# Performance work log

Measured on AMD Instinct MI355X. Metric: run time of the kernel, lower is better.

Reference implementation:

```python
import jax, jax.numpy as jnp
import numpy as np

B, N, M = 2, 2048, 1024
C, CTX, H = 1024, 1024, 16
D = C // H
HID = int(C * 4.0)
EPS = 1e-6


def _ln(h):
    # LayerNorm32: fp32 layernorm, eps=1e-6, no affine params
    h32 = h.astype(jnp.float32)
    mu = jnp.mean(h32, axis=-1, keepdims=True)
    var = jnp.var(h32, axis=-1, keepdims=True)
    return ((h32 - mu) * jax.lax.rsqrt(var + EPS)).astype(h.dtype)


def _sdpa(q, k, v):
    # q: [B,Q,H,D], k/v: [B,K,H,D]
    scale = 1.0 / np.sqrt(D)
    s = jnp.einsum('bqhd,bkhd->bhqk', q, k) * scale
    p = jax.nn.softmax(s, axis=-1)
    return jnp.einsum('bhqk,bkhd->bqhd', p, v)


def _forward(x, context, Wqkv, bqkv, Wos, bos, Wq, bq, Wkv, bkv, Woc, boc, W1, b1, W2, b2):
    Bx, Nx, _ = x.shape
    Mx = context.shape[1]
    # --- self-attention (attn_mode='full') ---
    h = _ln(x)
    qkv = (h @ Wqkv + bqkv).reshape(Bx, Nx, 3, H, D)
    q, k, v = qkv[:, :, 0], qkv[:, :, 1], qkv[:, :, 2]
    a = _sdpa(q, k, v).reshape(Bx, Nx, C)
    x = x + (a @ Wos + bos)
    # --- cross-attention (always 'full') ---
    h = _ln(x)
    q = (h @ Wq + bq).reshape(Bx, Nx, H, D)
    kv = (context @ Wkv + bkv).reshape(Bx, Mx, 2, H, D)
    k, v = kv[:, :, 0], kv[:, :, 1]
    a = _sdpa(q, k, v).reshape(Bx, Nx, C)
    x = x + (a @ Woc + boc)
    # --- FFN with tanh-approx GELU ---
    h = _ln(x)
    x = x + (jax.nn.gelu(h @ W1 + b1, approximate=True) @ W2 + b2)
    return x


def setup_inputs() -> dict:
    key = jax.random.key(0)
    ks = jax.random.split(key, 12)
    rn = lambda k, shape: (jax.random.normal(k, shape, jnp.float32) * 0.02)
    return {
        'x': jax.random.normal(ks[0], (B, N, C), jnp.float32),
        'context': jax.random.normal(ks[1], (B, M, CTX), jnp.float32),
        'Wqkv': rn(ks[2], (C, 3 * C)), 'bqkv': jnp.zeros((3 * C,), jnp.float32),
        'Wos': rn(ks[3], (C, C)), 'bos': jnp.zeros((C,), jnp.float32),
        'Wq': rn(ks[4], (C, C)), 'bq': jnp.zeros((C,), jnp.float32),
        'Wkv': rn(ks[5], (CTX, 2 * C)), 'bkv': jnp.zeros((2 * C,), jnp.float32),
        'Woc': rn(ks[6], (C, C)), 'boc': jnp.zeros((C,), jnp.float32),
        'W1': rn(ks[7], (C, HID)), 'b1': jnp.zeros((HID,), jnp.float32),
        'W2': rn(ks[8], (HID, C)), 'b2': jnp.zeros((C,), jnp.float32),
    }


def reference(x, context, Wqkv, bqkv, Wos, bos, Wq, bq, Wkv, bkv, Woc, boc, W1, b1, W2, b2):
    return _forward(x, context, Wqkv, bqkv, Wos, bos, Wq, bq, Wkv, bkv, Woc, boc, W1, b1, W2, b2)
```

## Files before the change

kernel.cpp:

```cpp
#include <hip/hip_runtime.h>
#include <cstdint>

typedef unsigned short u16;
typedef short bf16x8 __attribute__((ext_vector_type(8)));
typedef unsigned short u16x8 __attribute__((ext_vector_type(8)));
typedef float f32x4 __attribute__((ext_vector_type(4)));

__device__ __forceinline__ u16 f2bf(float f) {
  union { float f; uint32_t u; } v; v.f = f;
  uint32_t r = (v.u + 0x7fffu + ((v.u >> 16) & 1u)) >> 16;
  return (u16)r;
}

__device__ __forceinline__ void gload_lds16(const u16* g, u16* l) {
  __builtin_amdgcn_global_load_lds(
      (const __attribute__((address_space(1))) void*)g,
      (__attribute__((address_space(3))) void*)l, 16, 0, 0);
}

__global__ __launch_bounds__(256) void ln_kernel(const float* __restrict__ x,
                                                 u16* __restrict__ h) {
  const int row = blockIdx.x;
  const int tid = threadIdx.x;
  const float4 v = *reinterpret_cast<const float4*>(x + (long)row * 1024 + tid * 4);
  float s  = v.x + v.y + v.z + v.w;
  float ss = v.x * v.x + v.y * v.y + v.z * v.z + v.w * v.w;
#pragma unroll
  for (int off = 32; off >= 1; off >>= 1) {
    s  += __shfl_xor(s, off, 64);
    ss += __shfl_xor(ss, off, 64);
  }
  __shared__ float red[8];
  const int wave = tid >> 6, lane = tid & 63;
  if (lane == 0) { red[wave] = s; red[4 + wave] = ss; }
  __syncthreads();
  s  = red[0] + red[1] + red[2] + red[3];
  ss = red[4] + red[5] + red[6] + red[7];
  const float mu   = s * (1.0f / 1024.0f);
  const float var  = ss * (1.0f / 1024.0f) - mu * mu;
  const float rstd = rsqrtf(var + 1e-6f);
  ushort4 o;
  o.x = f2bf((v.x - mu) * rstd);
  o.y = f2bf((v.y - mu) * rstd);
  o.z = f2bf((v.z - mu) * rstd);
  o.w = f2bf((v.w - mu) * rstd);
  *reinterpret_cast<ushort4*>(h + (long)row * 1024 + tid * 4) = o;
}

struct WEnt { const float* W; u16* Wt; int K, N, tEnd; };
struct WEnts { WEnt e[7]; int n; };

__global__ __launch_bounds__(256) void wconvert_all(WEnts args) {
  __shared__ u16 tile[64][72];
  int t = blockIdx.x;
  int i = 0, tStart = 0;
  while (i < args.n - 1 && t >= args.e[i].tEnd) { tStart = args.e[i].tEnd; i++; }
  const float* W = args.e[i].W;
  u16* Wt = args.e[i].Wt;
  const int K = args.e[i].K, N = args.e[i].N;
  const int rel = t - tStart;
  const int ntn = N >> 6;
  const int tn = rel % ntn, tk = rel / ntn;
  const int n0 = tn * 64, k0 = tk * 64;

  const int th = threadIdx.x;
  const int c4 = (th & 15) * 4;
  const int r  = th >> 4;
#pragma unroll
  for (int ii = 0; ii < 4; ii++) {
    const int row = ii * 16 + r;
    const float4 v = *reinterpret_cast<const float4*>(W + (long)(k0 + row) * N + n0 + c4);
    tile[c4 + 0][row] = f2bf(v.x);
    tile[c4 + 1][row] = f2bf(v.y);
    tile[c4 + 2][row] = f2bf(v.z);
    tile[c4 + 3][row] = f2bf(v.w);
  }
  __syncthreads();
  const int c8 = (th & 7) * 8;
  const int rn = th >> 3;
#pragma unroll
  for (int ii = 0; ii < 2; ii++) {
    const int row = ii * 32 + rn;
    *reinterpret_cast<u16x8*>(Wt + (long)(n0 + row) * K + k0 + c8) =
        *reinterpret_cast<const u16x8*>(&tile[row][c8]);
  }
}

__global__ __launch_bounds__(256) void f2bf_kernel(const float* __restrict__ in,
                                                   u16* __restrict__ out) {
  const long i = ((long)blockIdx.x * 256 + threadIdx.x) * 4;
  const float4 v = *reinterpret_cast<const float4*>(in + i);
  ushort4 o;
  o.x = f2bf(v.x); o.y = f2bf(v.y); o.z = f2bf(v.z); o.w = f2bf(v.w);
  *reinterpret_cast<ushort4*>(out + i) = o;
}

__global__ __launch_bounds__(256) void vtrans(const u16* __restrict__ V,
                                              u16* __restrict__ Vt,
                                              int vStride, long vBatch, int nk) {
  __shared__ u16 tile[64][72];
  const int t = threadIdx.x;
  const int b = blockIdx.z, h = blockIdx.y, n0 = blockIdx.x * 64;
  const u16* vp = V + (long)b * vBatch + h * 64;
  u16* op = Vt + (long)(b * 16 + h) * 64 * (long)nk + n0;
  const int ch = t & 7;
#pragma unroll
  for (int i = 0; i < 2; i++) {
    const int n = (t >> 3) + i * 32;
    const u16x8 v = *reinterpret_cast<const u16x8*>(vp + (long)(n0 + n) * vStride + ch * 8);
#pragma unroll
    for (int j = 0; j < 8; j++) tile[ch * 8 + j][n] = v[j];
  }
  __syncthreads();
#pragma unroll
  for (int i = 0; i < 2; i++) {
    const int d = (t >> 3) + i * 32;
    *reinterpret_cast<u16x8*>(op + (long)d * nk + ch * 8) =
        *reinterpret_cast<const u16x8*>(&tile[d][ch * 8]);
  }
}

template <int TN, bool OUT_BF16, bool GELU_ACT, bool RES, int KSPLIT>
__device__ __forceinline__ void gemm_core(
    const u16* __restrict__ A, const u16* __restrict__ Bt,
    const float* __restrict__ bias, const float* __restrict__ res,
    void* __restrict__ Cout, int Ndim, int Kdim, int m0, int n0,
    u16* Al, u16* Bl) {
  constexpr int NFRAG = TN / 32;
  const int tid  = threadIdx.x;
  const int lane = tid & 63, wave = tid >> 6;
  const int quad = lane >> 4, l15 = lane & 15;
  const int wr = wave >> 1, wc = wave & 1;

  f32x4 acc[4][NFRAG];
  const f32x4 vzero = {0.f, 0.f, 0.f, 0.f};
#pragma unroll
  for (int i = 0; i < 4; i++)
#pragma unroll
    for (int jj = 0; jj < NFRAG; jj++) acc[i][jj] = vzero;

  const int Keff = Kdim / KSPLIT;
  const long kOff = (KSPLIT > 1) ? (long)blockIdx.y * Keff : 0;

  const long rowOff = (long)(lane >> 2) * Kdim + (((lane & 3) ^ ((lane >> 3) & 3)) * 8);
  const u16* gA = A  + (long)m0 * Kdim + rowOff + kOff;
  const u16* gB = Bt + (long)n0 * Kdim + rowOff + kOff;

  auto stage = [&](int k0, int p) {
    gload_lds16(gA + (long)(wave * 16) * Kdim + k0,       Al + p * 4096 + wave * 512);
    gload_lds16(gA + (long)((wave + 4) * 16) * Kdim + k0, Al + p * 4096 + (wave + 4) * 512);
    gload_lds16(gB + (long)(wave * 16) * Kdim + k0,       Bl + p * (TN * 32) + wave * 512);
    if constexpr (TN == 128)
      gload_lds16(gB + (long)((wave + 4) * 16) * Kdim + k0, Bl + p * (TN * 32) + (wave + 4) * 512);
  };

  const int swz = (quad ^ ((l15 >> 1) & 3)) * 8;

  stage(0, 0);
  int p = 0;
  for (int k0 = 0; k0 < Keff; k0 += 32, p ^= 1) {
    __syncthreads();
    bf16x8 af[4], bfr[NFRAG];
#pragma unroll
    for (int mt = 0; mt < 4; mt++)
      af[mt] = *reinterpret_cast<const bf16x8*>(Al + p * 4096 + (wr * 64 + mt * 16 + l15) * 32 + swz);
#pragma unroll
    for (int nt = 0; nt < NFRAG; nt++)
      bfr[nt] = *reinterpret_cast<const bf16x8*>(Bl + p * (TN * 32) + (wc * NFRAG * 16 + nt * 16 + l15) * 32 + swz);
    if (k0 + 32 < Keff) stage(k0 + 32, p ^ 1);
#pragma unroll
    for (int mt = 0; mt < 4; mt++)
#pragma unroll
      for (int nt = 0; nt < NFRAG; nt++)
        acc[mt][nt] = __builtin_amdgcn_mfma_f32_16x16x32_bf16(af[mt], bfr[nt], acc[mt][nt], 0, 0, 0);
  }

#pragma unroll
  for (int nt = 0; nt < NFRAG; nt++) {
    const int col = n0 + wc * NFRAG * 16 + nt * 16 + l15;
    const float bv = bias[col];
#pragma unroll
    for (int mt = 0; mt < 4; mt++) {
#pragma unroll
      for (int r = 0; r < 4; r++) {
        const int row = m0 + wr * 64 + mt * 16 + quad * 4 + r;
        if constexpr (KSPLIT > 1) {
          float y = acc[mt][nt][r];
          if (blockIdx.y == 0) y += bv;
          unsafeAtomicAdd(&((float*)Cout)[(long)row * Ndim + col], y);
        } else {
          float y = acc[mt][nt][r] + bv;
          if (GELU_ACT) {
            const float t = 0.7978845608028654f * (y + 0.044715f * y * y * y);
            y = 0.5f * y * (1.0f + tanhf(t));
          }
          if (RES) y += res[(long)row * Ndim + col];
          if (OUT_BF16)
            ((u16*)Cout)[(long)row * Ndim + col] = f2bf(y);
          else
            ((float*)Cout)[(long)row * Ndim + col] = y;
        }
      }
    }
  }
}

template <int TN, int SX, bool OUT_BF16, bool GELU_ACT, bool RES, int KSPLIT = 1>
__global__ __launch_bounds__(256, 2) void gemm_bt(
    const u16* __restrict__ A, const u16* __restrict__ Bt,
    const float* __restrict__ bias, const float* __restrict__ res,
    void* __restrict__ Cout, int Ndim, int Kdim, int lx, int ly) {
  __shared__ u16 Al[2 * 128 * 32];
  __shared__ u16 Bl[2 * TN * 32];
  const int j = blockIdx.x;
  const int c = j & 7, kk = j >> 3;
  const int cx = c % SX, cy = c / SX;
  const int bx = cx * lx + (kk % lx);
  const int by = cy * ly + (kk / lx);
  gemm_core<TN, OUT_BF16, GELU_ACT, RES, KSPLIT>(
      A, Bt, bias, res, Cout, Ndim, Kdim, by * 128, bx * TN, Al, Bl);
}

struct GemmSeg {
  const u16* A; const u16* Bt; const float* bias; u16* C;
  int Ndim, Kdim, SX, lx, ly;
};
struct GemmDualP { GemmSeg s0, s1; int nBlk0; };

template <int TN>
__global__ __launch_bounds__(256, 2) void gemm_dual(GemmDualP pp) {
  __shared__ u16 Al[2 * 128 * 32];
  __shared__ u16 Bl[2 * TN * 32];
  int j = blockIdx.x;
  GemmSeg s;
  if (j < pp.nBlk0) { s = pp.s0; } else { s = pp.s1; j -= pp.nBlk0; }
  const int c = j & 7, kk = j >> 3;
  const int cx = c % s.SX, cy = c / s.SX;
  const int bx = cx * s.lx + (kk % s.lx);
  const int by = cy * s.ly + (kk / s.lx);
  gemm_core<TN, true, false, false, 1>(
      s.A, s.Bt, s.bias, nullptr, s.C, s.Ndim, s.Kdim, by * 128, bx * TN, Al, Bl);
}

__global__ __launch_bounds__(256, 2) void attn_kernel(
    const u16* __restrict__ Q, const u16* __restrict__ K, const u16* __restrict__ Vt,
    u16* __restrict__ O, int nk, int qStride, int kStride, int oStride,
    long qBatch, long kBatch, long oBatch) {
  __shared__ u16 Kt[2][64 * 64];
  __shared__ u16 Vl[2][64 * 64];
  __shared__ u16 Pl[4][32 * 64];

  const int tid = threadIdx.x;
  const int lane = tid & 63, wave = tid >> 6;
  const int quad = lane >> 4, l15 = lane & 15;
  const int b = blockIdx.z, hh = blockIdx.y, qt = blockIdx.x;

  const u16* qp = Q + (long)b * qBatch + hh * 64;
  const u16* kp = K + (long)b * kBatch + hh * 64;
  const u16* vp = Vt + (long)(b * 16 + hh) * 64 * (long)nk;

  bf16x8 qf[2][2];
  const int qrow = qt * 128 + wave * 32 + l15;
#pragma unroll
  for (int qg = 0; qg < 2; qg++) {
    qf[qg][0] = *reinterpret_cast<const bf16x8*>(qp + (long)(qrow + qg * 16) * qStride + quad * 8);
    qf[qg][1] = *reinterpret_cast<const bf16x8*>(qp + (long)(qrow + qg * 16) * qStride + 32 + quad * 8);
  }

  const int r8 = lane >> 3;
  const int gcol = ((lane & 7) ^ r8) * 8;
  const u16* kgA = kp + (long)(wave * 8 + r8) * kStride + gcol;
  const u16* kgB = kp + (long)((wave + 4) * 8 + r8) * kStride + gcol;
  const u16* vgA = vp + (long)(wave * 8 + r8) * nk + gcol;
  const u16* vgB = vp + (long)((wave + 4) * 8 + r8) * nk + gcol;

  const int cF = (quad ^ (l15 & 7)) * 8;

  const f32x4 vzero = {0.f, 0.f, 0.f, 0.f};
  f32x4 oAcc[2][4];
  float lSt[2] = {0.f, 0.f};
#pragma unroll
  for (int qg = 0; qg < 2; qg++)
#pragma unroll
    for (int i = 0; i < 4; i++) oAcc[qg][i] = vzero;

  const float SCL = 0.18033688f;
  const int nTiles = nk >> 6;
  const long kAdv = (long)64 * kStride;

  auto stage = [&](int kt, int p) {
    gload_lds16(kgA + kt * kAdv, &Kt[p][wave * 512]);
    gload_lds16(kgB + kt * kAdv, &Kt[p][(wave + 4) * 512]);
    gload_lds16(vgA + kt * 64,   &Vl[p][wave * 512]);
    gload_lds16(vgB + kt * 64,   &Vl[p][(wave + 4) * 512]);
  };

  stage(0, 0);
  int p = 0;
  for (int kt = 0; kt < nTiles; kt++, p ^= 1) {
    __syncthreads();
    if (kt + 1 < nTiles) stage(kt + 1, p ^ 1);

    f32x4 st[2][4];
#pragma unroll
    for (int mt = 0; mt < 4; mt++) {
      const bf16x8 kf0 = *reinterpret_cast<const bf16x8*>(&Kt[p][(mt * 16 + l15) * 64 + cF]);
      const bf16x8 kf1 = *reinterpret_cast<const bf16x8*>(&Kt[p][(mt * 16 + l15) * 64 + (cF ^ 32)]);
#pragma unroll
      for (int qg = 0; qg < 2; qg++) {
        f32x4 z = vzero;
        z = __builtin_amdgcn_mfma_f32_16x16x32_bf16(kf0, qf[qg][0], z, 0, 0, 0);
        z = __builtin_amdgcn_mfma_f32_16x16x32_bf16(kf1, qf[qg][1], z, 0, 0, 0);
        st[qg][mt] = z;
      }
    }

#pragma unroll
    for (int qg = 0; qg < 2; qg++) {
      float ps = 0.f;
#pragma unroll
      for (int mt = 0; mt < 4; mt++)
#pragma unroll
        for (int r = 0; r < 4; r++) {
          const float pw = __builtin_amdgcn_exp2f(st[qg][mt][r] * SCL);
          st[qg][mt][r] = pw;
          ps += pw;
        }
      lSt[qg] += ps;
      u16* plw = &Pl[wave][(qg * 16 + l15) * 64];
#pragma unroll
      for (int mt = 0; mt < 4; mt++) {
        union { float f; uint32_t u; } a0, a1, a2, a3;
        a0.f = st[qg][mt][0]; a1.f = st[qg][mt][1];
        a2.f = st[qg][mt][2]; a3.f = st[qg][mt][3];
        a0.u += 0x8000u; a1.u += 0x8000u; a2.u += 0x8000u; a3.u += 0x8000u;
        uint2 w;
        w.x = __builtin_amdgcn_perm(a1.u, a0.u, 0x07060302u);
        w.y = __builtin_amdgcn_perm(a3.u, a2.u, 0x07060302u);
        const int pcol = (((mt * 2 + (quad >> 1)) ^ (l15 & 7)) * 8) + (quad & 1) * 4;
        *reinterpret_cast<uint2*>(&plw[pcol]) = w;
      }
    }

    bf16x8 pf[2][2];
#pragma unroll
    for (int qg = 0; qg < 2; qg++) {
      const u16* plw = &Pl[wave][(qg * 16 + l15) * 64];
      pf[qg][0] = *reinterpret_cast<const bf16x8*>(&plw[cF]);
      pf[qg][1] = *reinterpret_cast<const bf16x8*>(&plw[cF ^ 32]);
    }
#pragma unroll
    for (int dt = 0; dt < 4; dt++) {
      const bf16x8 vf0 = *reinterpret_cast<const bf16x8*>(&Vl[p][(dt * 16 + l15) * 64 + cF]);
      const bf16x8 vf1 = *reinterpret_cast<const bf16x8*>(&Vl[p][(dt * 16 + l15) * 64 + (cF ^ 32)]);
#pragma unroll
      for (int qg = 0; qg < 2; qg++) {
        oAcc[qg][dt] = __builtin_amdgcn_mfma_f32_16x16x32_bf16(pf[qg][0], vf0, oAcc[qg][dt], 0, 0, 0);
        oAcc[qg][dt] = __builtin_amdgcn_mfma_f32_16x16x32_bf16(pf[qg][1], vf1, oAcc[qg][dt], 0, 0, 0);
      }
    }
  }

  u16* op = O + (long)b * oBatch + hh * 64;
#pragma unroll
  for (int qg = 0; qg < 2; qg++) {
    float l = lSt[qg];
    l += __shfl_xor(l, 16, 64);
    l += __shfl_xor(l, 32, 64);
    float lR[4];
#pragma unroll
    for (int r = 0; r < 4; r++) lR[r] = 1.0f / __shfl(l, quad * 4 + r, 64);
#pragma unroll
    for (int dt = 0; dt < 4; dt++)
#pragma unroll
      for (int r = 0; r < 4; r++) {
        const int row = qt * 128 + wave * 32 + qg * 16 + quad * 4 + r;
        op[(long)row * oStride + dt * 16 + l15] = f2bf(oAcc[qg][dt][r] * lR[r]);
      }
  }
}

extern "C" void kernel_launch(void* const* d_in, const int* in_sizes, int n_in,
                              void* d_out, int out_size, void* d_ws, size_t ws_size,
                              hipStream_t stream) {
  const float* x    = (const float*)d_in[0];
  const float* ctx  = (const float*)d_in[1];
  const float* Wqkv = (const float*)d_in[2];
  const float* bqkv = (const float*)d_in[3];
  const float* Wos  = (const float*)d_in[4];
  const float* bos  = (const float*)d_in[5];
  const float* Wq   = (const float*)d_in[6];
  const float* bq   = (const float*)d_in[7];
  const float* Wkv  = (const float*)d_in[8];
  const float* bkv  = (const float*)d_in[9];
  const float* Woc  = (const float*)d_in[10];
  const float* boc  = (const float*)d_in[11];
  const float* W1   = (const float*)d_in[12];
  const float* b1   = (const float*)d_in[13];
  const float* W2   = (const float*)d_in[14];
  const float* b2   = (const float*)d_in[15];
  float* out = (float*)d_out;
  char* ws = (char*)d_ws;
  const size_t MB = 1024 * 1024;

  u16* h      = (u16*)ws;
  u16* abuf   = (u16*)(ws + 8 * MB);
  u16* wbuf   = (u16*)(ws + 8 * MB);
  u16* qkv    = (u16*)(ws + 16 * MB);
  u16* Wqkvt  = (u16*)(ws + 40 * MB);
  u16* Wost   = (u16*)(ws + 16 * MB);
  u16* Wqt    = (u16*)(ws + 18 * MB);
  u16* Wkvt   = (u16*)(ws + 20 * MB);
  u16* Woct   = (u16*)(ws + 24 * MB);
  u16* q2     = (u16*)(ws + 26 * MB);
  u16* kv2    = (u16*)(ws + 34 * MB);
  u16* ctxbf  = (u16*)(ws + 42 * MB);
  u16* VtCr   = (u16*)(ws + 16 * MB);
  u16* hid    = (u16*)(ws + 16 * MB);
  u16* VtSelf = h;
  u16* W1t    = wbuf;
  u16* W2t    = wbuf;

  WEnts w1; w1.n = 1;

  ln_kernel<<<dim3(4096), dim3(256), 0, stream>>>(x, h);
  w1.e[0] = {Wqkv, Wqkvt, 1024, 3072, 768};
  wconvert_all<<<dim3(768), dim3(256), 0, stream>>>(w1);
  gemm_bt<128, 2, true, false, false><<<dim3(768), dim3(256), 0, stream>>>(
      h, Wqkvt, bqkv, nullptr, qkv, 3072, 1024, 12, 8);
  vtrans<<<dim3(32, 16, 2), dim3(256), 0, stream>>>(
      qkv + 2048, VtSelf, 3072, (long)2048 * 3072, 2048);
  attn_kernel<<<dim3(16, 16, 2), dim3(256), 0, stream>>>(
      qkv, qkv + 1024, VtSelf, abuf, 2048, 3072, 3072, 1024,
      (long)2048 * 3072, (long)2048 * 3072, (long)2048 * 1024);

  WEnts w4; w4.n = 4;
  w4.e[0] = {Wos, Wost, 1024, 1024, 256};
  w4.e[1] = {Wq,  Wqt,  1024, 1024, 512};
  w4.e[2] = {Wkv, Wkvt, 1024, 2048, 1024};
  w4.e[3] = {Woc, Woct, 1024, 1024, 1280};
  wconvert_all<<<dim3(1280), dim3(256), 0, stream>>>(w4);
  f2bf_kernel<<<dim3(2048), dim3(256), 0, stream>>>(ctx, ctxbf);

  gemm_bt<64, 1, false, false, true><<<dim3(512), dim3(256), 0, stream>>>(
      abuf, Wost, bos, x, out, 1024, 1024, 16, 4);
  ln_kernel<<<dim3(4096), dim3(256), 0, stream>>>(out, h);

  GemmDualP dp;
  dp.s0 = {h,     Wqt,  bq,  q2,  1024, 1024, 1, 16, 4};
  dp.s1 = {ctxbf, Wkvt, bkv, kv2, 2048, 1024, 2, 16, 4};
  dp.nBlk0 = 512;
  gemm_dual<64><<<dim3(1024), dim3(256), 0, stream>>>(dp);
  vtrans<<<dim3(16, 16, 2), dim3(256), 0, stream>>>(
      kv2 + 1024, VtCr, 2048, (long)1024 * 2048, 1024);
  attn_kernel<<<dim3(16, 16, 2), dim3(256), 0, stream>>>(
      q2, kv2, VtCr, abuf, 1024, 1024, 2048, 1024,
      (long)2048 * 1024, (long)1024 * 2048, (long)2048 * 1024);
  gemm_bt<64, 1, false, false, false, 2><<<dim3(512, 2), dim3(256), 0, stream>>>(
      abuf, Woct, boc, nullptr, out, 1024, 1024, 16, 4);

  ln_kernel<<<dim3(4096), dim3(256), 0, stream>>>(out, h);
  w1.e[0] = {W1, W1t, 1024, 4096, 1024};
  wconvert_all<<<dim3(1024), dim3(256), 0, stream>>>(w1);
  gemm_bt<128, 2, true, true, false><<<dim3(1024), dim3(256), 0, stream>>>(
      h, W1t, b1, nullptr, hid, 4096, 1024, 16, 8);
  w1.e[0] = {W2, W2t, 4096, 1024, 1024};
  wconvert_all<<<dim3(1024), dim3(256), 0, stream>>>(w1);
  gemm_bt<128, 2, false, false, false, 4><<<dim3(256, 4), dim3(256), 0, stream>>>(
      hid, W2t, b2, nullptr, out, 1024, 4096, 4, 8);
}
```

Before: 520.9 us.

## Fuse layernorm with weight conversion, drop split-K atomics, use exp2 GELU

Merges the layernorm and weight-conversion launches into combined grids, and merges the context bf16 conversion with the weight-conversion launch, to cut launch count and let independent work overlap. Removes split-K with atomic adds for the cross-attention output projection and the FFN down projection. Those now use a single-pass 64-wide tile GEMM that adds the residual in place, which avoids atomic traffic but gives fewer blocks on the K=4096 GEMM. Replaces tanhf in GELU with an exp2-based sigmoid form.

```diff
diff --git a/kernel.cpp b/kernel.cpp
--- a/kernel.cpp
+++ b/kernel.cpp
@@ -18,9 +18,8 @@
       (__attribute__((address_space(3))) void*)l, 16, 0, 0);
 }
 
-__global__ __launch_bounds__(256) void ln_kernel(const float* __restrict__ x,
-                                                 u16* __restrict__ h) {
-  const int row = blockIdx.x;
+__device__ __forceinline__ void ln_body(const float* __restrict__ x,
+                                        u16* __restrict__ h, int row) {
   const int tid = threadIdx.x;
   const float4 v = *reinterpret_cast<const float4*>(x + (long)row * 1024 + tid * 4);
   float s  = v.x + v.y + v.z + v.w;
@@ -47,12 +46,16 @@
   *reinterpret_cast<ushort4*>(h + (long)row * 1024 + tid * 4) = o;
 }
 
+__global__ __launch_bounds__(256) void ln_kernel(const float* __restrict__ x,
+                                                 u16* __restrict__ h) {
+  ln_body(x, h, blockIdx.x);
+}
+
 struct WEnt { const float* W; u16* Wt; int K, N, tEnd; };
-struct WEnts { WEnt e[7]; int n; };
-
-__global__ __launch_bounds__(256) void wconvert_all(WEnts args) {
+struct WEnts { WEnt e[4]; int n; };
+
+__device__ __forceinline__ void wconv_body(const WEnts& args, int t) {
   __shared__ u16 tile[64][72];
-  int t = blockIdx.x;
   int i = 0, tStart = 0;
   while (i < args.n - 1 && t >= args.e[i].tEnd) { tStart = args.e[i].tEnd; i++; }
   const float* W = args.e[i].W;
@@ -86,13 +89,29 @@
   }
 }
 
-__global__ __launch_bounds__(256) void f2bf_kernel(const float* __restrict__ in,
-                                                   u16* __restrict__ out) {
-  const long i = ((long)blockIdx.x * 256 + threadIdx.x) * 4;
-  const float4 v = *reinterpret_cast<const float4*>(in + i);
-  ushort4 o;
-  o.x = f2bf(v.x); o.y = f2bf(v.y); o.z = f2bf(v.z); o.w = f2bf(v.w);
-  *reinterpret_cast<ushort4*>(out + i) = o;
+__global__ __launch_bounds__(256) void wconvert_all(WEnts args) {
+  wconv_body(args, blockIdx.x);
+}
+
+__global__ __launch_bounds__(256) void ln_wconv_combo(const float* __restrict__ x,
+                                                      u16* __restrict__ h, int nLn,
+                                                      WEnts args) {
+  if ((int)blockIdx.x < nLn) ln_body(x, h, blockIdx.x);
+  else                       wconv_body(args, blockIdx.x - nLn);
+}
+
+__global__ __launch_bounds__(256) void wconv_f2bf_combo(WEnts args, int nW,
+                                                        const float* __restrict__ in,
+                                                        u16* __restrict__ out) {
+  if ((int)blockIdx.x < nW) {
+    wconv_body(args, blockIdx.x);
+  } else {
+    const long i = ((long)(blockIdx.x - nW) * 256 + threadIdx.x) * 4;
+    const float4 v = *reinterpret_cast<const float4*>(in + i);
+    ushort4 o;
+    o.x = f2bf(v.x); o.y = f2bf(v.y); o.z = f2bf(v.z); o.w = f2bf(v.w);
+    *reinterpret_cast<ushort4*>(out + i) = o;
+  }
 }
 
 __global__ __launch_bounds__(256) void vtrans(const u16* __restrict__ V,
@@ -120,7 +139,7 @@
   }
 }
 
-template <int TN, bool OUT_BF16, bool GELU_ACT, bool RES, int KSPLIT>
+template <int TN, bool OUT_BF16, bool GELU_ACT, bool RES>
 __device__ __forceinline__ void gemm_core(
     const u16* __restrict__ A, const u16* __restrict__ Bt,
     const float* __restrict__ bias, const float* __restrict__ res,
@@ -139,12 +158,9 @@
 #pragma unroll
     for (int jj = 0; jj < NFRAG; jj++) acc[i][jj] = vzero;
 
-  const int Keff = Kdim / KSPLIT;
-  const long kOff = (KSPLIT > 1) ? (long)blockIdx.y * Keff : 0;
-
   const long rowOff = (long)(lane >> 2) * Kdim + (((lane & 3) ^ ((lane >> 3) & 3)) * 8);
-  const u16* gA = A  + (long)m0 * Kdim + rowOff + kOff;
-  const u16* gB = Bt + (long)n0 * Kdim + rowOff + kOff;
+  const u16* gA = A  + (long)m0 * Kdim + rowOff;
+  const u16* gB = Bt + (long)n0 * Kdim + rowOff;
 
   auto stage = [&](int k0, int p) {
     gload_lds16(gA + (long)(wave * 16) * Kdim + k0,       Al + p * 4096 + wave * 512);
@@ -158,7 +174,7 @@
 
   stage(0, 0);
   int p = 0;
-  for (int k0 = 0; k0 < Keff; k0 += 32, p ^= 1) {
+  for (int k0 = 0; k0 < Kdim; k0 += 32, p ^= 1) {
     __syncthreads();
     bf16x8 af[4], bfr[NFRAG];
 #pragma unroll
@@ -167,7 +183,7 @@
 #pragma unroll
     for (int nt = 0; nt < NFRAG; nt++)
       bfr[nt] = *reinterpret_cast<const bf16x8*>(Bl + p * (TN * 32) + (wc * NFRAG * 16 + nt * 16 + l15) * 32 + swz);
-    if (k0 + 32 < Keff) stage(k0 + 32, p ^ 1);
+    if (k0 + 32 < Kdim) stage(k0 + 32, p ^ 1);
 #pragma unroll
     for (int mt = 0; mt < 4; mt++)
 #pragma unroll
@@ -184,28 +200,22 @@
 #pragma unroll
       for (int r = 0; r < 4; r++) {
         const int row = m0 + wr * 64 + mt * 16 + quad * 4 + r;
-        if constexpr (KSPLIT > 1) {
-          float y = acc[mt][nt][r];
-          if (blockIdx.y == 0) y += bv;
-          unsafeAtomicAdd(&((float*)Cout)[(long)row * Ndim + col], y);
-        } else {
-          float y = acc[mt][nt][r] + bv;
-          if (GELU_ACT) {
-            const float t = 0.7978845608028654f * (y + 0.044715f * y * y * y);
-            y = 0.5f * y * (1.0f + tanhf(t));
-          }
-          if (RES) y += res[(long)row * Ndim + col];
-          if (OUT_BF16)
-            ((u16*)Cout)[(long)row * Ndim + col] = f2bf(y);
-          else
-            ((float*)Cout)[(long)row * Ndim + col] = y;
+        float y = acc[mt][nt][r] + bv;
+        if (GELU_ACT) {
+          const float t = 0.7978845608028654f * (y + 0.044715f * y * y * y);
+          y = y / (1.0f + __builtin_amdgcn_exp2f(-2.885390081777927f * t));
         }
+        if (RES) y += res[(long)row * Ndim + col];
+        if (OUT_BF16)
+          ((u16*)Cout)[(long)row * Ndim + col] = f2bf(y);
+        else
+          ((float*)Cout)[(long)row * Ndim + col] = y;
       }
     }
   }
 }
 
-template <int TN, int SX, bool OUT_BF16, bool GELU_ACT, bool RES, int KSPLIT = 1>
+template <int TN, int SX, bool OUT_BF16, bool GELU_ACT, bool RES>
 __global__ __launch_bounds__(256, 2) void gemm_bt(
     const u16* __restrict__ A, const u16* __restrict__ Bt,
     const float* __restrict__ bias, const float* __restrict__ res,
@@ -217,7 +227,7 @@
   const int cx = c % SX, cy = c / SX;
   const int bx = cx * lx + (kk % lx);
   const int by = cy * ly + (kk / lx);
-  gemm_core<TN, OUT_BF16, GELU_ACT, RES, KSPLIT>(
+  gemm_core<TN, OUT_BF16, GELU_ACT, RES>(
       A, Bt, bias, res, Cout, Ndim, Kdim, by * 128, bx * TN, Al, Bl);
 }
 
@@ -238,7 +248,7 @@
   const int cx = c % s.SX, cy = c / s.SX;
   const int bx = cx * s.lx + (kk % s.lx);
   const int by = cy * s.ly + (kk / s.lx);
-  gemm_core<TN, true, false, false, 1>(
+  gemm_core<TN, true, false, false>(
       s.A, s.Bt, s.bias, nullptr, s.C, s.Ndim, s.Kdim, by * 128, bx * TN, Al, Bl);
 }
 
@@ -423,9 +433,8 @@
 
   WEnts w1; w1.n = 1;
 
-  ln_kernel<<<dim3(4096), dim3(256), 0, stream>>>(x, h);
   w1.e[0] = {Wqkv, Wqkvt, 1024, 3072, 768};
-  wconvert_all<<<dim3(768), dim3(256), 0, stream>>>(w1);
+  ln_wconv_combo<<<dim3(4096 + 768), dim3(256), 0, stream>>>(x, h, 4096, w1);
   gemm_bt<128, 2, true, false, false><<<dim3(768), dim3(256), 0, stream>>>(
       h, Wqkvt, bqkv, nullptr, qkv, 3072, 1024, 12, 8);
   vtrans<<<dim3(32, 16, 2), dim3(256), 0, stream>>>(
@@ -439,8 +448,7 @@
   w4.e[1] = {Wq,  Wqt,  1024, 1024, 512};
   w4.e[2] = {Wkv, Wkvt, 1024, 2048, 1024};
   w4.e[3] = {Woc, Woct, 1024, 1024, 1280};
-  wconvert_all<<<dim3(1280), dim3(256), 0, stream>>>(w4);
-  f2bf_kernel<<<dim3(2048), dim3(256), 0, stream>>>(ctx, ctxbf);
+  wconv_f2bf_combo<<<dim3(1280 + 2048), dim3(256), 0, stream>>>(w4, 1280, ctx, ctxbf);
 
   gemm_bt<64, 1, false, false, true><<<dim3(512), dim3(256), 0, stream>>>(
       abuf, Wost, bos, x, out, 1024, 1024, 16, 4);
@@ -456,16 +464,15 @@
   attn_kernel<<<dim3(16, 16, 2), dim3(256), 0, stream>>>(
       q2, kv2, VtCr, abuf, 1024, 1024, 2048, 1024,
       (long)2048 * 1024, (long)1024 * 2048, (long)2048 * 1024);
-  gemm_bt<64, 1, false, false, false, 2><<<dim3(512, 2), dim3(256), 0, stream>>>(
-      abuf, Woct, boc, nullptr, out, 1024, 1024, 16, 4);
-
-  ln_kernel<<<dim3(4096), dim3(256), 0, stream>>>(out, h);
+  gemm_bt<64, 1, false, false, true><<<dim3(512), dim3(256), 0, stream>>>(
+      abuf, Woct, boc, out, out, 1024, 1024, 16, 4);
+
   w1.e[0] = {W1, W1t, 1024, 4096, 1024};
-  wconvert_all<<<dim3(1024), dim3(256), 0, stream>>>(w1);
+  ln_wconv_combo<<<dim3(4096 + 1024), dim3(256), 0, stream>>>(out, h, 4096, w1);
   gemm_bt<128, 2, true, true, false><<<dim3(1024), dim3(256), 0, stream>>>(
       h, W1t, b1, nullptr, hid, 4096, 1024, 16, 8);
   w1.e[0] = {W2, W2t, 4096, 1024, 1024};
   wconvert_all<<<dim3(1024), dim3(256), 0, stream>>>(w1);
-  gemm_bt<128, 2, false, false, false, 4><<<dim3(256, 4), dim3(256), 0, stream>>>(
-      hid, W2t, b2, nullptr, out, 1024, 4096, 4, 8);
-}
+  gemm_bt<64, 1, false, false, true><<<dim3(512), dim3(256), 0, stream>>>(
+      hid, W2t, b2, out, out, 1024, 4096, 16, 4);
+}
```

After: 468.1 us. -10.1%, faster.
